# Kernel optimization log

Measured on AMD Instinct MI355X. Metric: run time of the kernel, lower is better.

## Reference

```python
import jax, jax.numpy as jnp
import numpy as np

WINDOW_SIZE = 11
SIGMA = 1.5
C1 = 0.01 ** 2
C2 = 0.03 ** 2
LAMBDA_DSSIM = 0.2


def _gaussian_window(channel):
    x = jnp.arange(WINDOW_SIZE, dtype=jnp.float32)
    g = jnp.exp(-((x - WINDOW_SIZE // 2) ** 2) / (2.0 * SIGMA ** 2))
    g = g / g.sum()
    w2d = jnp.outer(g, g)  # [ws, ws]
    # depthwise kernel: [O=C, I=1, ws, ws]
    return jnp.broadcast_to(w2d[None, None], (channel, 1, WINDOW_SIZE, WINDOW_SIZE))


def _dwconv(x, window, channel):
    # x: [1, C, H, W]; same padding ws//2, depthwise (groups=C)
    pad = WINDOW_SIZE // 2
    return jax.lax.conv_general_dilated(
        x, window,
        window_strides=(1, 1),
        padding=((pad, pad), (pad, pad)),
        dimension_numbers=("NCHW", "OIHW", "NCHW"),
        feature_group_count=channel,
    )


def _ssim_mean(img1, img2):
    # img1, img2: [C, H, W]
    channel = img1.shape[0]
    window = _gaussian_window(channel).astype(img1.dtype)
    a = img1[None]  # [1, C, H, W]
    b = img2[None]

    mu1 = _dwconv(a, window, channel)
    mu2 = _dwconv(b, window, channel)
    mu1_sq = mu1 * mu1
    mu2_sq = mu2 * mu2
    mu1_mu2 = mu1 * mu2
    sigma1_sq = _dwconv(a * a, window, channel) - mu1_sq
    sigma2_sq = _dwconv(b * b, window, channel) - mu2_sq
    sigma12 = _dwconv(a * b, window, channel) - mu1_mu2

    ssim_map = ((2 * mu1_mu2 + C1) * (2 * sigma12 + C2)) / (
        (mu1_sq + mu2_sq + C1) * (sigma1_sq + sigma2_sq + C2))
    return ssim_map.mean()


def setup_inputs() -> dict:
    key = jax.random.key(0)
    k1, k2 = jax.random.split(key)
    shape = (3, 2160, 3840)
    pred = jax.random.uniform(k1, shape, dtype=jnp.float32)
    target = jax.random.uniform(k2, shape, dtype=jnp.float32)
    return {"pred": pred, "target": target}


def reference(pred, target):
    l1 = jnp.abs(pred - target).mean()
    ssim_val = _ssim_mean(pred, target)
    return (1.0 - LAMBDA_DSSIM) * l1 + LAMBDA_DSSIM * (1.0 - ssim_val)
```

## Files before the change

kernel.cpp:

```cpp
#include <hip/hip_runtime.h>
#include <math.h>

#define WSZ 11
#define PAD 5
#define TX 32
#define TY 24
#define NY 6
#define IY (TY + 2*PAD)
#define RX 4
#define NTASK0 (IY * 8)
#define NTASK1 (TY * 8)
#define SEG (RX + 2*PAD)
#define RY 3
#define SA 33

typedef float v2f __attribute__((ext_vector_type(2)));

struct W11 { float w[WSZ]; };

__global__ __launch_bounds__(256, 4) void ssim_l1_kernel(
    const float* __restrict__ pred, const float* __restrict__ targ,
    W11 wt, float2* __restrict__ partials)
{
    constexpr int H = 2160, W = 3840;
    __shared__ float4 sHA[IY][SA];

    const int c    = blockIdx.z;
    const int gx0  = blockIdx.x * TX;
    const int base = blockIdx.y * (TY * NY);
    const size_t plane = (size_t)H * W;
    const float* p = pred + (size_t)c * plane;
    const float* t = targ + (size_t)c * plane;

    const int tid = threadIdx.x;
    v2f loss_acc = {0.f, 0.f};
    const float C1v = 0.0001f, C2v = 0.0009f;

    const int oxB  = tid & 31;
    const int oy0B = (tid >> 5) * RY;
    const bool xfast = (blockIdx.x >= 1) && (blockIdx.x <= (W / TX) - 2);

    for (int s = 0; s < NY; ++s) {
        if (s > 0) {
            for (int i = tid; i < 2 * PAD * TX; i += 256) {
                const int dr = i >> 5, cc = i & 31;
                sHA[dr][cc] = sHA[dr + TY][cc];
            }
            __syncthreads();
        }

        const int ntask  = (s == 0) ? NTASK0 : NTASK1;
        const int rowoff = (s == 0) ? 0 : 2 * PAD;
        const int gyA    = base + TY * s - PAD;
        for (int task = tid; task < ntask; task += 256) {
            const int r  = task >> 3;
            const int cx = task & 7;
            const int rr = rowoff + r;
            const int gy = gyA + rr;
            const int gxs = gx0 + cx * RX - PAD;
            const bool rowok   = (gy >= 0) && (gy < H);
            const bool own_row = (gy >= base) && (gy < base + TY * NY);

            float4 P[5], T[5];
            if (rowok && xfast) {
                const float4* p4 = (const float4*)(p + (size_t)gy * W + (gxs - 3));
                const float4* t4 = (const float4*)(t + (size_t)gy * W + (gxs - 3));
                #pragma unroll
                for (int i = 0; i < 5; ++i) { P[i] = p4[i]; T[i] = t4[i]; }
            } else if (rowok) {
                const size_t rowoff2 = (size_t)gy * W;
                #pragma unroll
                for (int i = 0; i < 5; ++i) {
                    float pe[4], te[4];
                    #pragma unroll
                    for (int q = 0; q < 4; ++q) {
                        int gx = gxs - 3 + 4 * i + q;
                        bool ok = (gx >= 0) && (gx < W);
                        pe[q] = ok ? p[rowoff2 + gx] : 0.f;
                        te[q] = ok ? t[rowoff2 + gx] : 0.f;
                    }
                    P[i] = make_float4(pe[0], pe[1], pe[2], pe[3]);
                    T[i] = make_float4(te[0], te[1], te[2], te[3]);
                }
            } else {
                #pragma unroll
                for (int i = 0; i < 5; ++i) {
                    P[i] = make_float4(0.f, 0.f, 0.f, 0.f);
                    T[i] = make_float4(0.f, 0.f, 0.f, 0.f);
                }
            }

            v2f h_sd[RX], h_qq[RX];
            #pragma unroll
            for (int j = 0; j < RX; ++j) {
                h_sd[j] = (v2f){0.f, 0.f};
                h_qq[j] = (v2f){0.f, 0.f};
            }
            #pragma unroll
            for (int e = 0; e < SEG; ++e) {
                const int ii = (e + 3) >> 2, qq = (e + 3) & 3;
                const float pe = (qq == 0) ? P[ii].x : (qq == 1) ? P[ii].y
                                : (qq == 2) ? P[ii].z : P[ii].w;
                const float te = (qq == 0) ? T[ii].x : (qq == 1) ? T[ii].y
                                : (qq == 2) ? T[ii].z : T[ii].w;
                v2f vsd; vsd.x = pe + te; vsd.y = pe - te;
                const v2f vsq = vsd * vsd;
                #pragma unroll
                for (int j = 0; j < RX; ++j) {
                    const int k = e - j;
                    if (k >= 0 && k < WSZ) {
                        const float wv = wt.w[k];
                        h_sd[j] += wv * vsd;
                        h_qq[j] += wv * vsq;
                    }
                }
                if (e >= PAD && e < PAD + RX && own_row)
                    loss_acc.y += fabsf(vsd.y);
            }
            const int xb = cx * RX;
            #pragma unroll
            for (int j = 0; j < RX; ++j)
                sHA[rr][xb + j] = make_float4(h_sd[j].x, h_sd[j].y,
                                              h_qq[j].x, h_qq[j].y);
        }
        __syncthreads();

        {
            v2f mu[RY], qq[RY];
            #pragma unroll
            for (int j = 0; j < RY; ++j) {
                mu[j] = (v2f){0.f, 0.f};
                qq[j] = (v2f){0.f, 0.f};
            }
            #pragma unroll
            for (int k = 0; k < RY + 2 * PAD; ++k) {
                const float4 f = sHA[oy0B + k][oxB];
                v2f fsd; fsd.x = f.x; fsd.y = f.y;
                v2f fsq; fsq.x = f.z; fsq.y = f.w;
                #pragma unroll
                for (int j = 0; j < RY; ++j) {
                    const int kk = k - j;
                    if (kk >= 0 && kk < WSZ) {
                        const float wv = wt.w[kk];
                        mu[j] += wv * fsd;
                        qq[j] += wv * fsq;
                    }
                }
            }
            #pragma unroll
            for (int j = 0; j < RY; ++j) {
                const v2f musq = mu[j] * mu[j];
                const v2f rr2  = qq[j] - musq;
                const float a  = 0.5f * (musq.x - musq.y) + C1v;
                const float b  = 0.5f * (rr2.x - rr2.y) + C2v;
                const float cden = 0.5f * (musq.x + musq.y) + C1v;
                const float dden = 0.5f * (rr2.x + rr2.y) + C2v;
                loss_acc.x += (a * b) * __builtin_amdgcn_rcpf(cden * dden);
            }
        }
        __syncthreads();
    }

    #pragma unroll
    for (int off = 32; off > 0; off >>= 1) {
        loss_acc.x += __shfl_down(loss_acc.x, off, 64);
        loss_acc.y += __shfl_down(loss_acc.y, off, 64);
    }
    __shared__ float red[2][4];
    const int lane = tid & 63;
    const int wid  = tid >> 6;
    if (lane == 0) { red[0][wid] = loss_acc.x; red[1][wid] = loss_acc.y; }
    __syncthreads();
    if (tid == 0) {
        const float sv = red[0][0] + red[0][1] + red[0][2] + red[0][3];
        const float lv = red[1][0] + red[1][1] + red[1][2] + red[1][3];
        const int bid = (blockIdx.z * gridDim.y + blockIdx.y) * gridDim.x + blockIdx.x;
        partials[bid] = make_float2(sv, lv);
    }
}

__global__ __launch_bounds__(256) void finalize_kernel(
    const float2* __restrict__ partials, int n,
    float* __restrict__ out, double invN)
{
    const int tid = threadIdx.x;
    double s = 0.0, l = 0.0;
    for (int i = tid; i < n; i += 256) {
        float2 v = partials[i];
        s += (double)v.x;
        l += (double)v.y;
    }
    #pragma unroll
    for (int off = 32; off > 0; off >>= 1) {
        s += __shfl_down(s, off, 64);
        l += __shfl_down(l, off, 64);
    }
    __shared__ double rs[4], rl[4];
    const int lane = tid & 63, wid = tid >> 6;
    if (lane == 0) { rs[wid] = s; rl[wid] = l; }
    __syncthreads();
    if (tid == 0) {
        const double st = rs[0] + rs[1] + rs[2] + rs[3];
        const double lt = rl[0] + rl[1] + rl[2] + rl[3];
        out[0] = (float)(0.8 * lt * invN + 0.2 * (1.0 - st * invN));
    }
}

extern "C" void kernel_launch(void* const* d_in, const int* in_sizes, int n_in,
                              void* d_out, int out_size, void* d_ws, size_t ws_size,
                              hipStream_t stream)
{
    const float* pred = (const float*)d_in[0];
    const float* targ = (const float*)d_in[1];
    float* out = (float*)d_out;
    float2* partials = (float2*)d_ws;

    const int C = 3, H = 2160, W = 3840;

    W11 wt;
    double g[WSZ], sg = 0.0;
    for (int i = 0; i < WSZ; ++i) {
        double d = (double)i - (WSZ / 2);
        g[i] = exp(-(d * d) / (2.0 * 1.5 * 1.5));
        sg += g[i];
    }
    for (int i = 0; i < WSZ; ++i) wt.w[i] = (float)(g[i] / sg);

    dim3 grid(W / TX, H / (TY * NY), C);
    ssim_l1_kernel<<<grid, 256, 0, stream>>>(pred, targ, wt, partials);

    const int nblocks = (W / TX) * (H / (TY * NY)) * C;
    double invN = 1.0 / ((double)C * (double)H * (double)W);
    finalize_kernel<<<1, 256, 0, stream>>>(partials, nblocks, out, invN);
}
```

Baseline: 246.8 us.

## Prefetch next strip's global loads into registers during vertical pass

Issues the global float4 loads for the next row strip's horizontal pass into registers before the vertical convolution of the current strip, so memory latency overlaps with compute. The task loop is restructured into lambdas, with the first task per thread using the prefetched registers. This adds 40 live registers of prefetch state, which could hurt occupancy under launch_bounds(256,4) or cause spills.

```diff
diff --git a/kernel.cpp b/kernel.cpp
--- a/kernel.cpp
+++ b/kernel.cpp
@@ -40,6 +40,102 @@
     const int oy0B = (tid >> 5) * RY;
     const bool xfast = (blockIdx.x >= 1) && (blockIdx.x <= (W / TX) - 2);
 
+    float4 PF_P[5], PF_T[5];
+
+    auto issue_pf = [&](const int s) {
+        const int ntask = (s == 0) ? NTASK0 : NTASK1;
+        const int rowoff = (s == 0) ? 0 : 2 * PAD;
+        const int r  = tid >> 3;
+        const int cx = tid & 7;
+        const int gy = base + TY * s - PAD + rowoff + r;
+        const int gxs = gx0 + cx * RX - PAD;
+        if (tid < ntask && gy >= 0 && gy < H && xfast) {
+            const float4* p4 = (const float4*)(p + (size_t)gy * W + (gxs - 3));
+            const float4* t4 = (const float4*)(t + (size_t)gy * W + (gxs - 3));
+            #pragma unroll
+            for (int i = 0; i < 5; ++i) { PF_P[i] = p4[i]; PF_T[i] = t4[i]; }
+        }
+    };
+
+    auto do_task = [&](const int task, const int s, const bool use_pf) {
+        const int r  = task >> 3;
+        const int cx = task & 7;
+        const int rr = ((s == 0) ? 0 : 2 * PAD) + r;
+        const int gy = base + TY * s - PAD + rr;
+        const int gxs = gx0 + cx * RX - PAD;
+        const bool rowok   = (gy >= 0) && (gy < H);
+        const bool own_row = (gy >= base) && (gy < base + TY * NY);
+
+        float4 P[5], T[5];
+        if (rowok && xfast) {
+            if (use_pf) {
+                #pragma unroll
+                for (int i = 0; i < 5; ++i) { P[i] = PF_P[i]; T[i] = PF_T[i]; }
+            } else {
+                const float4* p4 = (const float4*)(p + (size_t)gy * W + (gxs - 3));
+                const float4* t4 = (const float4*)(t + (size_t)gy * W + (gxs - 3));
+                #pragma unroll
+                for (int i = 0; i < 5; ++i) { P[i] = p4[i]; T[i] = t4[i]; }
+            }
+        } else if (rowok) {
+            const size_t rowoff2 = (size_t)gy * W;
+            #pragma unroll
+            for (int i = 0; i < 5; ++i) {
+                float pe[4], te[4];
+                #pragma unroll
+                for (int q = 0; q < 4; ++q) {
+                    int gx = gxs - 3 + 4 * i + q;
+                    bool ok = (gx >= 0) && (gx < W);
+                    pe[q] = ok ? p[rowoff2 + gx] : 0.f;
+                    te[q] = ok ? t[rowoff2 + gx] : 0.f;
+                }
+                P[i] = make_float4(pe[0], pe[1], pe[2], pe[3]);
+                T[i] = make_float4(te[0], te[1], te[2], te[3]);
+            }
+        } else {
+            #pragma unroll
+            for (int i = 0; i < 5; ++i) {
+                P[i] = make_float4(0.f, 0.f, 0.f, 0.f);
+                T[i] = make_float4(0.f, 0.f, 0.f, 0.f);
+            }
+        }
+
+        v2f h_sd[RX], h_qq[RX];
+        #pragma unroll
+        for (int j = 0; j < RX; ++j) {
+            h_sd[j] = (v2f){0.f, 0.f};
+            h_qq[j] = (v2f){0.f, 0.f};
+        }
+        #pragma unroll
+        for (int e = 0; e < SEG; ++e) {
+            const int ii = (e + 3) >> 2, qq = (e + 3) & 3;
+            const float pe = (qq == 0) ? P[ii].x : (qq == 1) ? P[ii].y
+                            : (qq == 2) ? P[ii].z : P[ii].w;
+            const float te = (qq == 0) ? T[ii].x : (qq == 1) ? T[ii].y
+                            : (qq == 2) ? T[ii].z : T[ii].w;
+            v2f vsd; vsd.x = pe + te; vsd.y = pe - te;
+            const v2f vsq = vsd * vsd;
+            #pragma unroll
+            for (int j = 0; j < RX; ++j) {
+                const int k = e - j;
+                if (k >= 0 && k < WSZ) {
+                    const float wv = wt.w[k];
+                    h_sd[j] += wv * vsd;
+                    h_qq[j] += wv * vsq;
+                }
+            }
+            if (e >= PAD && e < PAD + RX && own_row)
+                loss_acc.y += fabsf(vsd.y);
+        }
+        const int xb = cx * RX;
+        #pragma unroll
+        for (int j = 0; j < RX; ++j)
+            sHA[rr][xb + j] = make_float4(h_sd[j].x, h_sd[j].y,
+                                          h_qq[j].x, h_qq[j].y);
+    };
+
+    issue_pf(0);
+
     for (int s = 0; s < NY; ++s) {
         if (s > 0) {
             for (int i = tid; i < 2 * PAD * TX; i += 256) {
@@ -49,81 +145,14 @@
             __syncthreads();
         }
 
-        const int ntask  = (s == 0) ? NTASK0 : NTASK1;
-        const int rowoff = (s == 0) ? 0 : 2 * PAD;
-        const int gyA    = base + TY * s - PAD;
-        for (int task = tid; task < ntask; task += 256) {
-            const int r  = task >> 3;
-            const int cx = task & 7;
-            const int rr = rowoff + r;
-            const int gy = gyA + rr;
-            const int gxs = gx0 + cx * RX - PAD;
-            const bool rowok   = (gy >= 0) && (gy < H);
-            const bool own_row = (gy >= base) && (gy < base + TY * NY);
-
-            float4 P[5], T[5];
-            if (rowok && xfast) {
-                const float4* p4 = (const float4*)(p + (size_t)gy * W + (gxs - 3));
-                const float4* t4 = (const float4*)(t + (size_t)gy * W + (gxs - 3));
-                #pragma unroll
-                for (int i = 0; i < 5; ++i) { P[i] = p4[i]; T[i] = t4[i]; }
-            } else if (rowok) {
-                const size_t rowoff2 = (size_t)gy * W;
-                #pragma unroll
-                for (int i = 0; i < 5; ++i) {
-                    float pe[4], te[4];
-                    #pragma unroll
-                    for (int q = 0; q < 4; ++q) {
-                        int gx = gxs - 3 + 4 * i + q;
-                        bool ok = (gx >= 0) && (gx < W);
-                        pe[q] = ok ? p[rowoff2 + gx] : 0.f;
-                        te[q] = ok ? t[rowoff2 + gx] : 0.f;
-                    }
-                    P[i] = make_float4(pe[0], pe[1], pe[2], pe[3]);
-                    T[i] = make_float4(te[0], te[1], te[2], te[3]);
-                }
-            } else {
-                #pragma unroll
-                for (int i = 0; i < 5; ++i) {
-                    P[i] = make_float4(0.f, 0.f, 0.f, 0.f);
-                    T[i] = make_float4(0.f, 0.f, 0.f, 0.f);
-                }
-            }
-
-            v2f h_sd[RX], h_qq[RX];
-            #pragma unroll
-            for (int j = 0; j < RX; ++j) {
-                h_sd[j] = (v2f){0.f, 0.f};
-                h_qq[j] = (v2f){0.f, 0.f};
-            }
-            #pragma unroll
-            for (int e = 0; e < SEG; ++e) {
-                const int ii = (e + 3) >> 2, qq = (e + 3) & 3;
-                const float pe = (qq == 0) ? P[ii].x : (qq == 1) ? P[ii].y
-                                : (qq == 2) ? P[ii].z : P[ii].w;
-                const float te = (qq == 0) ? T[ii].x : (qq == 1) ? T[ii].y
-                                : (qq == 2) ? T[ii].z : T[ii].w;
-                v2f vsd; vsd.x = pe + te; vsd.y = pe - te;
-                const v2f vsq = vsd * vsd;
-                #pragma unroll
-                for (int j = 0; j < RX; ++j) {
-                    const int k = e - j;
-                    if (k >= 0 && k < WSZ) {
-                        const float wv = wt.w[k];
-                        h_sd[j] += wv * vsd;
-                        h_qq[j] += wv * vsq;
-                    }
-                }
-                if (e >= PAD && e < PAD + RX && own_row)
-                    loss_acc.y += fabsf(vsd.y);
-            }
-            const int xb = cx * RX;
-            #pragma unroll
-            for (int j = 0; j < RX; ++j)
-                sHA[rr][xb + j] = make_float4(h_sd[j].x, h_sd[j].y,
-                                              h_qq[j].x, h_qq[j].y);
+        {
+            const int ntask = (s == 0) ? NTASK0 : NTASK1;
+            if (tid < ntask) do_task(tid, s, true);
+            if (s == 0 && tid < NTASK0 - 256) do_task(tid + 256, 0, false);
         }
         __syncthreads();
+
+        if (s + 1 < NY) issue_pf(s + 1);
 
         {
             v2f mu[RY], qq[RY];
@@ -151,8 +180,8 @@
             for (int j = 0; j < RY; ++j) {
                 const v2f musq = mu[j] * mu[j];
                 const v2f rr2  = qq[j] - musq;
-                const float a  = 0.5f * (musq.x - musq.y) + C1v;
-                const float b  = 0.5f * (rr2.x - rr2.y) + C2v;
+                const float a    = 0.5f * (musq.x - musq.y) + C1v;
+                const float b    = 0.5f * (rr2.x - rr2.y) + C2v;
                 const float cden = 0.5f * (musq.x + musq.y) + C1v;
                 const float dden = 0.5f * (rr2.x + rr2.y) + C2v;
                 loss_acc.x += (a * b) * __builtin_amdgcn_rcpf(cden * dden);
```

Measured after the change: 288.5 us. +16.9%, slower.
